# Optimization experiments

Measured on AMD Instinct MI355X. Metric: run time of the kernel, lower is better.

## Reference

```python
import jax, jax.numpy as jnp
import numpy as np

D_SUMMARY = 128
N_LAYERS = 24
N_HEADS = 16
D_HEAD = 64
HIDDEN = 512
ACTIVE_MIN = 12
ROT = 16
THETA = 10000.0
B, P = 16, 128
L_ACT = N_LAYERS - ACTIVE_MIN
OUT_DIM = N_HEADS * 2 * D_HEAD


def setup_inputs() -> dict:
    key = jax.random.key(0)
    k1, k2, k3, k4, k5, k6 = jax.random.split(key, 6)
    summary_stack = jax.random.normal(k1, (B, P, D_SUMMARY), jnp.float32)
    positions = jnp.sort(jax.random.randint(k2, (P,), 0, 8192))
    s1 = 1.0 / np.sqrt(D_SUMMARY)
    s2 = 1.0 / np.sqrt(HIDDEN)
    W1 = jax.random.uniform(k3, (L_ACT, D_SUMMARY, HIDDEN), jnp.float32, -s1, s1)
    b1 = jax.random.uniform(k4, (L_ACT, HIDDEN), jnp.float32, -s1, s1)
    W2 = jax.random.uniform(k5, (L_ACT, HIDDEN, OUT_DIM), jnp.float32, -s2, s2)
    b2 = jax.random.uniform(k6, (L_ACT, OUT_DIM), jnp.float32, -s2, s2)
    return {"summary_stack": summary_stack, "positions": positions,
            "W1": W1, "b1": b1, "W2": W2, "b2": b2}


def reference(summary_stack, positions, W1, b1, W2, b2):
    # Batched 2-layer MLP across all active layers (grouped GEMM)
    h = jax.nn.relu(jnp.einsum('bps,lsh->lbph', summary_stack, W1) + b1[:, None, None, :])
    kv = jnp.einsum('lbph,lho->lbpo', h, W2) + b2[:, None, None, :]
    kv = kv.reshape(L_ACT, B, P, N_HEADS, 2, D_HEAD)
    k = jnp.transpose(kv[..., 0, :], (0, 1, 3, 2, 4))  # (L,B,H,P,D)
    v = jnp.transpose(kv[..., 1, :], (0, 1, 3, 2, 4))
    # RoPE on first ROT dims of K
    inv_freq = 1.0 / (THETA ** (jnp.arange(0, ROT, 2, dtype=jnp.float32) / ROT))
    freqs = positions.astype(jnp.float32)[:, None] * inv_freq[None, :]  # (P, ROT//2)
    emb = jnp.concatenate([freqs, freqs], axis=-1)  # (P, ROT)
    cos, sin = jnp.cos(emb), jnp.sin(emb)
    k_rot, k_pass = k[..., :ROT], k[..., ROT:]
    rot_half = jnp.concatenate([-k_rot[..., ROT // 2:], k_rot[..., :ROT // 2]], axis=-1)
    k_emb = k_rot * cos + rot_half * sin
    k = jnp.concatenate([k_emb, k_pass], axis=-1)
    # Inactive layers get zero K/V
    zeros = jnp.zeros((ACTIVE_MIN, B, N_HEADS, P, D_HEAD), k.dtype)
    k_all = jnp.concatenate([zeros, k], axis=0)
    v_all = jnp.concatenate([zeros, v], axis=0)
    return jnp.stack([k_all, v_all], axis=1)  # (n_layers, 2, B, H, P, D)
```

## Files before the change

kernel.cpp:

```cpp
#include <hip/hip_runtime.h>
#include <hip/hip_bf16.h>

#define L_ACT   12
#define BDIM    16
#define PDIM    128
#define DSUM    128
#define HID     512
#define ODIM    2048
#define NHEAD   16
#define DHEAD   64
#define MROWS   2048

typedef short s16x4  __attribute__((ext_vector_type(4)));
typedef short short8 __attribute__((ext_vector_type(8)));
typedef float f32x4  __attribute__((ext_vector_type(4)));

__device__ __forceinline__ void gload_lds16(const __hip_bfloat16* g, __hip_bfloat16* l) {
  __builtin_amdgcn_global_load_lds(
      (const __attribute__((address_space(1))) unsigned int*)g,
      (__attribute__((address_space(3))) unsigned int*)l, 16, 0, 0);
}

__device__ __forceinline__ short f2bf(float x) {
  __hip_bfloat16 h = __float2bfloat16(x);
  return *reinterpret_cast<short*>(&h);
}

__global__ __launch_bounds__(256) void zerofill_kernel(f32x4* __restrict__ p, int n16) {
  int stride = gridDim.x * 256;
  for (int i = blockIdx.x * 256 + threadIdx.x; i < n16; i += stride)
    p[i] = {0.f, 0.f, 0.f, 0.f};
}

__global__ __launch_bounds__(256) void prep_tiny(
    const int* __restrict__ positions, const float* __restrict__ W1,
    float* __restrict__ cs, __hip_bfloat16* __restrict__ W1T) {
  const int bid = blockIdx.x;
  const int tid = threadIdx.x;
  if (bid == 768) {
#pragma unroll
    for (int q = 0; q < 4; ++q) {
      int i = q * 256 + tid;
      int p = i >> 3, f = i & 7;
      double inv = pow(10000.0, -(double)f / 8.0);
      double ang = (double)positions[p] * inv;
      cs[i]        = (float)cos(ang);
      cs[1024 + i] = (float)sin(ang);
    }
  } else {
    __shared__ float t[32][33];
    int bx = bid & 15, by = (bid >> 4) & 3, l = bid >> 6;
    int o0 = bx * 32, j0 = by * 32;
    int tx = tid & 31, ty = tid >> 5;
    const float* ip = W1 + (size_t)l * DSUM * HID;
#pragma unroll
    for (int r = 0; r < 32; r += 8)
      t[ty + r][tx] = ip[(size_t)(j0 + ty + r) * HID + o0 + tx];
    __syncthreads();
    __hip_bfloat16* op = W1T + (size_t)l * DSUM * HID;
#pragma unroll
    for (int r = 0; r < 32; r += 8)
      op[(size_t)(o0 + ty + r) * DSUM + j0 + tx] = __float2bfloat16(t[tx][ty + r]);
  }
}

__global__ __launch_bounds__(256) void gemm1_128(
    const float* __restrict__ summary,
    const __hip_bfloat16* __restrict__ Ball,
    const float* __restrict__ bias,
    __hip_bfloat16* __restrict__ Hall,
    const float* __restrict__ W2,
    __hip_bfloat16* __restrict__ W2T,
    f32x4* __restrict__ zeroBase, int doZero) {
  const int KTOT = DSUM, NTOT = HID;
  __shared__ __hip_bfloat16 shbuf[17408];
  __hip_bfloat16* ldsA = shbuf;
  __hip_bfloat16* ldsB = shbuf + 8192;
  const int l    = blockIdx.z;
  const int n0   = blockIdx.x * 128;
  const int m0   = blockIdx.y * 128;
  const int tid  = threadIdx.x;
  const int wid  = tid >> 6;
  const int lane = tid & 63;
  const int wr = wid >> 1, wc = wid & 1;
  const __hip_bfloat16* Bt = Ball + (size_t)l * NTOT * KTOT;

  f32x4 acc[4][4];
#pragma unroll
  for (int m = 0; m < 4; ++m)
#pragma unroll
    for (int n = 0; n < 4; ++n)
      acc[m][n] = {0.f, 0.f, 0.f, 0.f};

  const int srowi = lane >> 3;
  const int sblk  = (lane & 7) ^ srowi;

  for (int kt = 0; kt < KTOT / 64; ++kt) {
    __syncthreads();
#pragma unroll
    for (int s = 0; s < 4; ++s) {
      int seg = wid * 4 + s;
      int row = seg * 8 + srowi;
      gload_lds16(Bt + (size_t)(n0 + row) * KTOT + kt * 64 + sblk * 8, ldsB + seg * 512);
    }
#pragma unroll
    for (int j = 0; j < 8; ++j) {
      int s = j * 256 + tid;
      int r = s >> 4, g = s & 15;
      f32x4 v = *(const f32x4*)(summary + (size_t)(m0 + r) * DSUM + kt * 64 + g * 4);
      s16x4 w;
      w[0] = f2bf(v[0]); w[1] = f2bf(v[1]); w[2] = f2bf(v[2]); w[3] = f2bf(v[3]);
      int ch = g >> 1;
      *(s16x4*)((char*)ldsA + r * 128 + ((ch ^ (r & 7)) << 4) + (g & 1) * 8) = w;
    }
    __syncthreads();
#pragma unroll
    for (int kk = 0; kk < 2; ++kk) {
      short8 af[4], bfr[4];
#pragma unroll
      for (int m = 0; m < 4; ++m) {
        int row = wr * 64 + m * 16 + (lane & 15);
        int off = (kk * 64 + (lane >> 4) * 16) ^ ((row & 7) << 4);
        af[m] = *(const short8*)((const char*)ldsA + row * 128 + off);
      }
#pragma unroll
      for (int n = 0; n < 4; ++n) {
        int row = wc * 64 + n * 16 + (lane & 15);
        int off = (kk * 64 + (lane >> 4) * 16) ^ ((row & 7) << 4);
        bfr[n] = *(const short8*)((const char*)ldsB + row * 128 + off);
      }
#pragma unroll
      for (int m = 0; m < 4; ++m)
#pragma unroll
        for (int n = 0; n < 4; ++n)
          acc[m][n] = __builtin_amdgcn_mfma_f32_16x16x32_bf16(af[m], bfr[n], acc[m][n], 0, 0, 0);
    }
  }

  const int bid = blockIdx.x + 4 * blockIdx.y + 64 * blockIdx.z;

  __syncthreads();
#pragma unroll
  for (int n = 0; n < 4; ++n) {
    int col = wc * 64 + n * 16 + (lane & 15);
    float bb = bias[l * NTOT + n0 + col];
#pragma unroll
    for (int m = 0; m < 4; ++m) {
      int rowb = wr * 64 + m * 16 + ((lane >> 4) << 2);
#pragma unroll
      for (int j = 0; j < 4; ++j) {
        float v = acc[m][n][j] + bb;
        v = v > 0.f ? v : 0.f;
        shbuf[(rowb + j) * 136 + col] = __float2bfloat16(v);
      }
    }
  }
  __syncthreads();
  {
    __hip_bfloat16* H = Hall + (size_t)l * MROWS * HID;
#pragma unroll
    for (int i = 0; i < 8; ++i) {
      int idx = i * 256 + tid;
      int row = idx >> 4, seg = idx & 15;
      short8 v = *(const short8*)(shbuf + row * 136 + seg * 8);
      *(short8*)(H + (size_t)(m0 + row) * HID + n0 + seg * 8) = v;
    }
  }

  {
    float* tb0 = (float*)shbuf;
    float* tb1 = (float*)shbuf + 1056;
    const int tx = tid & 31, ty = tid >> 5;
    const int tbase = bid * 16;
    const f32x4 z = {0.f, 0.f, 0.f, 0.f};
    f32x4* zp = zeroBase + (size_t)bid * 16384;
    float rvA0, rvA1, rvA2, rvA3, rvB0, rvB1, rvB2, rvB3;

#define W2_LOAD(P, tt_) do {                                                \
      int t_ = tbase + (tt_);                                               \
      int lz_ = t_ >> 10, rem_ = t_ & 1023;                                 \
      int j0_ = (rem_ >> 6) * 32, o0_ = (rem_ & 63) * 32;                   \
      const float* ip_ = W2 + (size_t)lz_ * HID * ODIM                      \
                       + (size_t)(j0_ + ty) * ODIM + o0_ + tx;              \
      P##0 = ip_[0];                                                        \
      P##1 = ip_[(size_t)8 * ODIM];                                         \
      P##2 = ip_[(size_t)16 * ODIM];                                        \
      P##3 = ip_[(size_t)24 * ODIM];                                        \
    } while (0)

#define W2_WRITE(buf, P) do {                                               \
      (buf)[(ty +  0) * 33 + tx] = P##0;                                    \
      (buf)[(ty +  8) * 33 + tx] = P##1;                                    \
      (buf)[(ty + 16) * 33 + tx] = P##2;                                    \
      (buf)[(ty + 24) * 33 + tx] = P##3;                                    \
    } while (0)

#define W2_STORE(buf, tt_) do {                                             \
      int t_ = tbase + (tt_);                                               \
      int lz_ = t_ >> 10, rem_ = t_ & 1023;                                 \
      int j0_ = (rem_ >> 6) * 32, o0_ = (rem_ & 63) * 32;                   \
      __hip_bfloat16* op_ = W2T + (size_t)lz_ * HID * ODIM;                 \
      _Pragma("unroll")                                                     \
      for (int r_ = 0; r_ < 4; ++r_)                                        \
        op_[(size_t)(o0_ + ty + 8 * r_) * HID + j0_ + tx] =                 \
            __float2bfloat16((buf)[tx * 33 + ty + 8 * r_]);                 \
    } while (0)

#define ZCHUNK(tt_) do { if (doZero && (tt_) < 11) {                        \
      _Pragma("unroll")                                                     \
      for (int q_ = 0; q_ < 4; ++q_)                                        \
        __builtin_nontemporal_store(z, zp + ((tt_) * 4 + q_) * 256 + tid);  \
    } } while (0)

    W2_LOAD(rvA, 0);
    W2_LOAD(rvB, 1);
    W2_WRITE(tb0, rvA);
    __syncthreads();
#pragma unroll 1
    for (int tt = 0; tt < 16; tt += 2) {
      if (tt + 2 < 16) W2_LOAD(rvA, tt + 2);
      W2_STORE(tb0, tt);
      W2_WRITE(tb1, rvB);
      ZCHUNK(tt);
      __syncthreads();
      if (tt + 3 < 16) W2_LOAD(rvB, tt + 3);
      W2_STORE(tb1, tt + 1);
      if (tt + 2 < 16) W2_WRITE(tb0, rvA);
      ZCHUNK(tt + 1);
      __syncthreads();
    }
#undef W2_LOAD
#undef W2_WRITE
#undef W2_STORE
#undef ZCHUNK
  }
}

__global__ __launch_bounds__(512, 1) void gemm2_pipe(
    const __hip_bfloat16* __restrict__ Aall,
    const __hip_bfloat16* __restrict__ Ball,
    const float* __restrict__ bias,
    const float* __restrict__ cs,
    float* __restrict__ O,
    f32x4* __restrict__ zeroBase, int doZero) {
  __shared__ __hip_bfloat16 lds[4 * 16384];
  const int orig = blockIdx.x + 8 * blockIdx.y + 64 * blockIdx.z;
  const int nw   = (orig & 7) * 96 + (orig >> 3);
  const int bx   = nw & 7;
  const int by   = (nw >> 3) & 7;
  const int l    = nw >> 6;
  const int n0  = bx * 256;
  const int m0  = by * 256;
  const int tid = threadIdx.x;
  const int wid = tid >> 6, lane = tid & 63;
  const int wm  = wid >> 2, wn = wid & 3;
  const __hip_bfloat16* A  = Aall + (size_t)l * MROWS * HID;
  const __hip_bfloat16* Bt = Ball + (size_t)l * ODIM * HID;
  f32x4* zq = zeroBase + (size_t)nw * 16384 + 11264;
  const f32x4 zv = {0.f, 0.f, 0.f, 0.f};

  f32x4 acc[8][4];
#pragma unroll
  for (int m = 0; m < 8; ++m)
#pragma unroll
    for (int n = 0; n < 4; ++n)
      acc[m][n] = {0.f, 0.f, 0.f, 0.f};

  const int cidx0 = wid * 128 + lane;
  const int cidx1 = cidx0 + 64;
  const int r0 = cidx0 >> 2, c0 = (cidx0 & 3) ^ ((r0 >> 1) & 3);
  const int r1 = cidx1 >> 2, c1 = (cidx1 & 3) ^ ((r1 >> 1) & 3);

#define STAGE_A(slot, kt) do {                                                      \
    gload_lds16(A + (size_t)(m0 + r0) * HID + (kt) * 32 + c0 * 8,                   \
                lds + (slot) * 16384 + wid * 1024);                                 \
    gload_lds16(A + (size_t)(m0 + r1) * HID + (kt) * 32 + c1 * 8,                   \
                lds + (slot) * 16384 + wid * 1024 + 512);                           \
  } while (0)
#define STAGE_B(slot, kt) do {                                                      \
    gload_lds16(Bt + (size_t)(n0 + r0) * HID + (kt) * 32 + c0 * 8,                  \
                lds + (slot) * 16384 + 8192 + wid * 1024);                          \
    gload_lds16(Bt + (size_t)(n0 + r1) * HID + (kt) * 32 + c1 * 8,                  \
                lds + (slot) * 16384 + 8192 + wid * 1024 + 512);                    \
  } while (0)

  const int kq   = lane >> 4;
  const int rl15 = lane & 15;

#define LD_FRAG(dst, base, rr) do {                                                 \
    int r_ = (rr);                                                                  \
    int off_ = r_ * 64 + ((kq ^ ((r_ >> 1) & 3)) << 4);                             \
    dst = *(const short8*)((const char*)(base) + off_);                             \
  } while (0)

  STAGE_A(0, 0); STAGE_B(0, 0);
  STAGE_A(1, 1); STAGE_B(1, 1);
  STAGE_A(2, 2); STAGE_B(2, 2);
  asm volatile("s_waitcnt vmcnt(8)" ::: "memory");
  __builtin_amdgcn_s_barrier();

  const int NT = HID / 32;
  for (int t = 0; t < NT; ++t) {
    const __hip_bfloat16* sa = lds + (t & 3) * 16384;
    const __hip_bfloat16* sb = sa + 8192;
    short8 af[4], bfr[4];

    if (doZero && t < 10)
      __builtin_nontemporal_store(zv, zq + t * 512 + tid);

#pragma unroll
    for (int n = 0; n < 4; ++n) LD_FRAG(bfr[n], sb, wn * 64 + n * 16 + rl15);
#pragma unroll
    for (int mi = 0; mi < 4; ++mi) LD_FRAG(af[mi], sa, wm * 128 + mi * 16 + rl15);
    if (t + 3 < NT) STAGE_A((t + 3) & 3, t + 3);
    __builtin_amdgcn_s_barrier();
    __builtin_amdgcn_s_setprio(1);
#pragma unroll
    for (int mi = 0; mi < 4; ++mi)
#pragma unroll
      for (int n = 0; n < 4; ++n)
        acc[mi][n] = __builtin_amdgcn_mfma_f32_16x16x32_bf16(af[mi], bfr[n], acc[mi][n], 0, 0, 0);
    __builtin_amdgcn_s_setprio(0);
    __builtin_amdgcn_s_barrier();

#pragma unroll
    for (int mi = 0; mi < 4; ++mi) LD_FRAG(af[mi], sa, wm * 128 + 64 + mi * 16 + rl15);
    if (t + 3 < NT) STAGE_B((t + 3) & 3, t + 3);
    __builtin_amdgcn_s_barrier();
    __builtin_amdgcn_s_setprio(1);
#pragma unroll
    for (int mi = 0; mi < 4; ++mi)
#pragma unroll
      for (int n = 0; n < 4; ++n)
        acc[4 + mi][n] = __builtin_amdgcn_mfma_f32_16x16x32_bf16(af[mi], bfr[n], acc[4 + mi][n], 0, 0, 0);
    __builtin_amdgcn_s_setprio(0);
    if (t < NT - 1) {
      if (t <= NT - 4)      asm volatile("s_waitcnt vmcnt(8)" ::: "memory");
      else if (t == NT - 3) asm volatile("s_waitcnt vmcnt(4)" ::: "memory");
      else                  asm volatile("s_waitcnt vmcnt(0)" ::: "memory");
    }
    __builtin_amdgcn_s_barrier();
  }
#undef STAGE_A
#undef STAGE_B
#undef LD_FRAG

  __syncthreads();
  const int head = bx * 2 + (wn >> 1);
  const int tkv  = wn & 1;
  const int bidx = by * 2 + wm;
  float* slab = O + ((((size_t)(l + L_ACT) * 2 + tkv) * BDIM + bidx) * NHEAD + head) * (PDIM * DHEAD);
  const bool ropeWave = (tkv == 0);

  float bb[4];
#pragma unroll
  for (int n = 0; n < 4; ++n) bb[n] = bias[l * ODIM + n0 + wn * 64 + n * 16 + rl15];

  float* Tw = (float*)lds + wid * 2080;

#pragma unroll
  for (int c = 0; c < 4; ++c) {
#pragma unroll
    for (int mh = 0; mh < 2; ++mh) {
      int mf = c * 2 + mh;
      int pl = mh * 16 + (lane >> 4) * 4;
#pragma unroll
      for (int n = 0; n < 4; ++n) {
#pragma unroll
        for (int j = 0; j < 4; ++j) {
          float v = acc[mf][n][j] + bb[n];
          if (ropeWave && n == 0) {
            float partner = __shfl_xor(v, 8);
            int p = c * 32 + pl + j;
            float cv = cs[p * 8 + (lane & 7)];
            float sv = cs[1024 + p * 8 + (lane & 7)];
            v = v * cv + (((lane & 15) < 8) ? -partner : partner) * sv;
          }
          Tw[(pl + j) * 65 + n * 16 + rl15] = v;
        }
      }
    }
#pragma unroll
    for (int it = 0; it < 8; ++it) {
      int pl = it * 4 + (lane >> 4);
      f32x4 vv = *(const f32x4*)(Tw + pl * 65 + rl15 * 4);
      __builtin_nontemporal_store(vv, (f32x4*)(slab + (size_t)(c * 32 + pl) * DHEAD + rl15 * 4));
    }
  }
}

extern "C" void kernel_launch(void* const* d_in, const int* in_sizes, int n_in,
                              void* d_out, int out_size, void* d_ws, size_t ws_size,
                              hipStream_t stream) {
  const float* summary   = (const float*)d_in[0];
  const int*   positions = (const int*)d_in[1];
  const float* W1 = (const float*)d_in[2];
  const float* b1 = (const float*)d_in[3];
  const float* W2 = (const float*)d_in[4];
  const float* b2 = (const float*)d_in[5];
  float* out = (float*)d_out;

  const size_t SCRATCH_BYTES = 25165824ULL + 25165824ULL + 1572864ULL + 8192ULL;
  const bool useWs = (ws_size >= SCRATCH_BYTES);
  char* sc = useWs ? (char*)d_ws : (char*)d_out;
  __hip_bfloat16* h_bf = (__hip_bfloat16*)sc;
  __hip_bfloat16* W2T  = (__hip_bfloat16*)(sc + 25165824);
  __hip_bfloat16* W1T  = (__hip_bfloat16*)(sc + 50331648);
  float*          cs   = (float*)(sc + 51904512);

  prep_tiny<<<769, 256, 0, stream>>>(positions, W1, cs, W1T);

  gemm1_128<<<dim3(HID / 128, MROWS / 128, L_ACT), 256, 0, stream>>>(
      summary, W1T, b1, h_bf, W2, W2T, (f32x4*)d_out, useWs ? 1 : 0);
  gemm2_pipe<<<dim3(ODIM / 256, MROWS / 256, L_ACT), 512, 0, stream>>>(
      h_bf, W2T, b2, cs, out, (f32x4*)d_out, useWs ? 1 : 0);

  if (!useWs)
    zerofill_kernel<<<2048, 256, 0, stream>>>((f32x4*)d_out, 12582912);
}
```

Measured before the change: 127.8 us.

## Shrink gemm2 tile to 256x128 with 4 waves, 3-stage pipeline, 2 blocks/CU

Reworks the second GEMM from 512-thread blocks with 256x256 tiles and a 4-slot LDS ring to 256-thread blocks with 256x128 tiles and a 3-slot ring, allowing two blocks per CU and twice as many blocks. The zero-fill of inactive layers is repartitioned: gemm2 blocks now zero the first half of the output, and gemm1 blocks zero the rest from an offset base. The goal is better latency hiding through occupancy and more even load balance. The trade-off is less prefetch depth and less reuse of each B tile, since each block now covers only one head.

```diff
diff --git a/kernel.cpp b/kernel.cpp
--- a/kernel.cpp
+++ b/kernel.cpp
@@ -173,7 +173,7 @@
     const int tx = tid & 31, ty = tid >> 5;
     const int tbase = bid * 16;
     const f32x4 z = {0.f, 0.f, 0.f, 0.f};
-    f32x4* zp = zeroBase + (size_t)bid * 16384;
+    f32x4* zp = zeroBase + (size_t)bid * 8192;
     float rvA0, rvA1, rvA2, rvA3, rvB0, rvB1, rvB2, rvB3;
 
 #define W2_LOAD(P, tt_) do {                                                \
@@ -206,7 +206,7 @@
             __float2bfloat16((buf)[tx * 33 + ty + 8 * r_]);                 \
     } while (0)
 
-#define ZCHUNK(tt_) do { if (doZero && (tt_) < 11) {                        \
+#define ZCHUNK(tt_) do { if (doZero && (tt_) < 8) {                         \
       _Pragma("unroll")                                                     \
       for (int q_ = 0; q_ < 4; ++q_)                                        \
         __builtin_nontemporal_store(z, zp + ((tt_) * 4 + q_) * 256 + tid);  \
@@ -236,27 +236,27 @@
   }
 }
 
-__global__ __launch_bounds__(512, 1) void gemm2_pipe(
+__global__ __launch_bounds__(256, 2) void gemm2_pipe(
     const __hip_bfloat16* __restrict__ Aall,
     const __hip_bfloat16* __restrict__ Ball,
     const float* __restrict__ bias,
     const float* __restrict__ cs,
     float* __restrict__ O,
     f32x4* __restrict__ zeroBase, int doZero) {
-  __shared__ __hip_bfloat16 lds[4 * 16384];
-  const int orig = blockIdx.x + 8 * blockIdx.y + 64 * blockIdx.z;
-  const int nw   = (orig & 7) * 96 + (orig >> 3);
-  const int bx   = nw & 7;
-  const int by   = (nw >> 3) & 7;
-  const int l    = nw >> 6;
-  const int n0  = bx * 256;
+  __shared__ __hip_bfloat16 lds[3 * 12288];
+  const int orig = blockIdx.x + 16 * blockIdx.y + 128 * blockIdx.z;
+  const int nw   = (orig & 7) * 192 + (orig >> 3);
+  const int bx   = nw & 15;
+  const int by   = (nw >> 4) & 7;
+  const int l    = nw >> 7;
+  const int n0  = bx * 128;
   const int m0  = by * 256;
   const int tid = threadIdx.x;
   const int wid = tid >> 6, lane = tid & 63;
-  const int wm  = wid >> 2, wn = wid & 3;
+  const int wm  = wid >> 1, wn = wid & 1;
   const __hip_bfloat16* A  = Aall + (size_t)l * MROWS * HID;
   const __hip_bfloat16* Bt = Ball + (size_t)l * ODIM * HID;
-  f32x4* zq = zeroBase + (size_t)nw * 16384 + 11264;
+  f32x4* zq = zeroBase + (size_t)nw * 4096;
   const f32x4 zv = {0.f, 0.f, 0.f, 0.f};
 
   f32x4 acc[8][4];
@@ -266,22 +266,29 @@
     for (int n = 0; n < 4; ++n)
       acc[m][n] = {0.f, 0.f, 0.f, 0.f};
 
-  const int cidx0 = wid * 128 + lane;
-  const int cidx1 = cidx0 + 64;
-  const int r0 = cidx0 >> 2, c0 = (cidx0 & 3) ^ ((r0 >> 1) & 3);
-  const int r1 = cidx1 >> 2, c1 = (cidx1 & 3) ^ ((r1 >> 1) & 3);
+  int ra[4], ca[4], rb[2], cb[2];
+#pragma unroll
+  for (int j = 0; j < 4; ++j) {
+    int cx = j * 256 + tid;
+    ra[j] = cx >> 2; ca[j] = (cx & 3) ^ ((ra[j] >> 1) & 3);
+  }
+#pragma unroll
+  for (int j = 0; j < 2; ++j) {
+    int cx = j * 256 + tid;
+    rb[j] = cx >> 2; cb[j] = (cx & 3) ^ ((rb[j] >> 1) & 3);
+  }
 
 #define STAGE_A(slot, kt) do {                                                      \
-    gload_lds16(A + (size_t)(m0 + r0) * HID + (kt) * 32 + c0 * 8,                   \
-                lds + (slot) * 16384 + wid * 1024);                                 \
-    gload_lds16(A + (size_t)(m0 + r1) * HID + (kt) * 32 + c1 * 8,                   \
-                lds + (slot) * 16384 + wid * 1024 + 512);                           \
+    _Pragma("unroll")                                                               \
+    for (int j_ = 0; j_ < 4; ++j_)                                                  \
+      gload_lds16(A + (size_t)(m0 + ra[j_]) * HID + (kt) * 32 + ca[j_] * 8,         \
+                  lds + (slot) * 12288 + j_ * 2048 + wid * 512);                    \
   } while (0)
 #define STAGE_B(slot, kt) do {                                                      \
-    gload_lds16(Bt + (size_t)(n0 + r0) * HID + (kt) * 32 + c0 * 8,                  \
-                lds + (slot) * 16384 + 8192 + wid * 1024);                          \
-    gload_lds16(Bt + (size_t)(n0 + r1) * HID + (kt) * 32 + c1 * 8,                  \
-                lds + (slot) * 16384 + 8192 + wid * 1024 + 512);                    \
+    _Pragma("unroll")                                                               \
+    for (int j_ = 0; j_ < 2; ++j_)                                                  \
+      gload_lds16(Bt + (size_t)(n0 + rb[j_]) * HID + (kt) * 32 + cb[j_] * 8,        \
+                  lds + (slot) * 12288 + 8192 + j_ * 2048 + wid * 512);             \
   } while (0)
 
   const int kq   = lane >> 4;
@@ -295,24 +302,24 @@
 
   STAGE_A(0, 0); STAGE_B(0, 0);
   STAGE_A(1, 1); STAGE_B(1, 1);
-  STAGE_A(2, 2); STAGE_B(2, 2);
-  asm volatile("s_waitcnt vmcnt(8)" ::: "memory");
+  asm volatile("s_waitcnt vmcnt(6)" ::: "memory");
   __builtin_amdgcn_s_barrier();
 
   const int NT = HID / 32;
   for (int t = 0; t < NT; ++t) {
-    const __hip_bfloat16* sa = lds + (t & 3) * 16384;
+    const int cur = t % 3;
+    const __hip_bfloat16* sa = lds + cur * 12288;
     const __hip_bfloat16* sb = sa + 8192;
     short8 af[4], bfr[4];
 
-    if (doZero && t < 10)
-      __builtin_nontemporal_store(zv, zq + t * 512 + tid);
+    if (doZero)
+      __builtin_nontemporal_store(zv, zq + t * 256 + tid);
 
 #pragma unroll
     for (int n = 0; n < 4; ++n) LD_FRAG(bfr[n], sb, wn * 64 + n * 16 + rl15);
 #pragma unroll
     for (int mi = 0; mi < 4; ++mi) LD_FRAG(af[mi], sa, wm * 128 + mi * 16 + rl15);
-    if (t + 3 < NT) STAGE_A((t + 3) & 3, t + 3);
+    if (t + 2 < NT) STAGE_A((t + 2) % 3, t + 2);
     __builtin_amdgcn_s_barrier();
     __builtin_amdgcn_s_setprio(1);
 #pragma unroll
@@ -325,7 +332,7 @@
 
 #pragma unroll
     for (int mi = 0; mi < 4; ++mi) LD_FRAG(af[mi], sa, wm * 128 + 64 + mi * 16 + rl15);
-    if (t + 3 < NT) STAGE_B((t + 3) & 3, t + 3);
+    if (t + 2 < NT) STAGE_B((t + 2) % 3, t + 2);
     __builtin_amdgcn_s_barrier();
     __builtin_amdgcn_s_setprio(1);
 #pragma unroll
@@ -334,11 +341,8 @@
       for (int n = 0; n < 4; ++n)
         acc[4 + mi][n] = __builtin_amdgcn_mfma_f32_16x16x32_bf16(af[mi], bfr[n], acc[4 + mi][n], 0, 0, 0);
     __builtin_amdgcn_s_setprio(0);
-    if (t < NT - 1) {
-      if (t <= NT - 4)      asm volatile("s_waitcnt vmcnt(8)" ::: "memory");
-      else if (t == NT - 3) asm volatile("s_waitcnt vmcnt(4)" ::: "memory");
-      else                  asm volatile("s_waitcnt vmcnt(0)" ::: "memory");
-    }
+    if (t < NT - 2)       asm volatile("s_waitcnt vmcnt(6)" ::: "memory");
+    else if (t == NT - 2) asm volatile("s_waitcnt vmcnt(0)" ::: "memory");
     __builtin_amdgcn_s_barrier();
   }
 #undef STAGE_A
@@ -346,8 +350,8 @@
 #undef LD_FRAG
 
   __syncthreads();
-  const int head = bx * 2 + (wn >> 1);
-  const int tkv  = wn & 1;
+  const int head = bx;
+  const int tkv  = wn;
   const int bidx = by * 2 + wm;
   float* slab = O + ((((size_t)(l + L_ACT) * 2 + tkv) * BDIM + bidx) * NHEAD + head) * (PDIM * DHEAD);
   const bool ropeWave = (tkv == 0);
@@ -411,8 +415,9 @@
   prep_tiny<<<769, 256, 0, stream>>>(positions, W1, cs, W1T);
 
   gemm1_128<<<dim3(HID / 128, MROWS / 128, L_ACT), 256, 0, stream>>>(
-      summary, W1T, b1, h_bf, W2, W2T, (f32x4*)d_out, useWs ? 1 : 0);
-  gemm2_pipe<<<dim3(ODIM / 256, MROWS / 256, L_ACT), 512, 0, stream>>>(
+      summary, W1T, b1, h_bf, W2, W2T,
+      (f32x4*)((char*)d_out + 100663296), useWs ? 1 : 0);
+  gemm2_pipe<<<dim3(ODIM / 128, MROWS / 256, L_ACT), 256, 0, stream>>>(
       h_bf, W2T, b2, cs, out, (f32x4*)d_out, useWs ? 1 : 0);
 
   if (!useWs)
```

Result: no change. 126.7 us (-0.9%).
